# Kernel optimization log

Measured on AMD Instinct MI355X. Metric: run time of the kernel, lower is better.

The kernel has to match this reference:

```python
import jax, jax.numpy as jnp
import numpy as np

H, KV, D, WIN = 16, 4, 128, 1024


def _rope(x, cos, sin):
    # x: [B, H, S, D]; cos/sin: [1, 1, S, D//2]
    d = x.shape[-1] // 2
    x1, x2 = x[..., :d], x[..., d:]
    S = x.shape[2]
    c, s = cos[:, :, :S], sin[:, :, :S]
    return jnp.concatenate([x1 * c + x2 * s, -x1 * s + x2 * c], axis=-1)


def _rms_norm(x):
    eps = jnp.finfo(x.dtype).eps
    return x * jax.lax.rsqrt(jnp.mean(jnp.square(x), axis=-1, keepdims=True) + eps)


def setup_inputs() -> dict:
    key = jax.random.key(0)
    ks = jax.random.split(key, 7)
    B, S, E = 2, 2048, 2048
    return {
        "x": jax.random.normal(ks[0], (B, S, E), jnp.float32),
        "cos": jax.random.normal(ks[1], (1, 1, S, D // 2), jnp.float32),
        "sin": jax.random.normal(ks[2], (1, 1, S, D // 2), jnp.float32),
        "Wq": jax.random.normal(ks[3], (H * D, E), jnp.float32) * 0.02,
        "Wk": jax.random.normal(ks[4], (KV * D, E), jnp.float32) * 0.02,
        "Wv": jax.random.normal(ks[5], (KV * D, E), jnp.float32) * 0.02,
        "Wo": jax.random.normal(ks[6], (E, H * D), jnp.float32) * 0.02,
    }


def reference(x, cos, sin, Wq, Wk, Wv, Wo):
    B, S, E = x.shape
    rep = H // KV
    # projections -> [B, heads, S, D]
    q = (x @ Wq.T).reshape(B, S, H, D).transpose(0, 2, 1, 3)
    k = (x @ Wk.T).reshape(B, S, KV, D).transpose(0, 2, 1, 3)
    v = (x @ Wv.T).reshape(B, S, KV, D).transpose(0, 2, 1, 3)
    # GQA: materialize repeated K/V heads (matches repeat_interleave)
    k = jnp.repeat(k, rep, axis=1)
    v = jnp.repeat(v, rep, axis=1)
    # RoPE then QK RMSNorm (no learned scale)
    q = _rms_norm(_rope(q, cos, sin))
    k = _rms_norm(_rope(k, cos, sin))
    scores = jnp.einsum("bhqd,bhkd->bhqk", q, k) * (D ** -0.5)
    # causal & sliding-window mask
    i = jnp.arange(S)[:, None]
    j = jnp.arange(S)[None, :]
    mask = (i >= j) & (jnp.abs(i - j) < WIN)
    scores = jnp.where(mask[None, None], scores, -jnp.inf)
    attn = jax.nn.softmax(scores, axis=-1)
    out = jnp.einsum("bhqk,bhkd->bhqd", attn, v)
    out = out.transpose(0, 2, 1, 3).reshape(B, S, H * D)
    return out @ Wo.T
```

## Files before the change

### kernel.cpp

```cpp
#include <hip/hip_runtime.h>
#include <stdint.h>

using bf16 = __bf16;
typedef __bf16 bf16x8 __attribute__((ext_vector_type(8)));
typedef __bf16 bf16x4 __attribute__((ext_vector_type(4)));
typedef float f32x4 __attribute__((ext_vector_type(4)));

#define H_ 16
#define KV_ 4
#define D_ 128
#define WIN_ 1024
#define B_ 2
#define S_ 2048
#define E_ 2048
#define HD_ 2048

__device__ __forceinline__ void gld_lds16(const void* gptr, void* lptr) {
    __builtin_amdgcn_global_load_lds(
        (__attribute__((address_space(1))) void*)(uintptr_t)gptr,
        (__attribute__((address_space(3))) void*)(uintptr_t)lptr, 16, 0, 0);
}

__global__ __launch_bounds__(256) void cvt_all(const float* __restrict__ x,
                                               const float* __restrict__ wq,
                                               const float* __restrict__ wk,
                                               const float* __restrict__ wv,
                                               const float* __restrict__ wo,
                                               bf16* __restrict__ dst) {
    int i = (blockIdx.x * 256 + threadIdx.x) * 4;
    const float* src;
    int off;
    if (i < 8388608)       { src = x;  off = 0; }
    else if (i < 12582912) { src = wq; off = 8388608; }
    else if (i < 13631488) { src = wk; off = 12582912; }
    else if (i < 14680064) { src = wv; off = 13631488; }
    else                   { src = wo; off = 14680064; }
    const float4 v = *(const float4*)(src + (i - off));
    bf16x4 o = {(bf16)v.x, (bf16)v.y, (bf16)v.z, (bf16)v.w};
    *(bf16x4*)(dst + i) = o;
}


template <typename OutT>
__global__ __launch_bounds__(256) void gemm_bt(const bf16* __restrict__ A,
                                               const bf16* __restrict__ W,
                                               OutT* __restrict__ C, int K, int ldc) {
    __shared__ alignas(16) bf16 As[128 * 64];
    __shared__ alignas(16) bf16 Bs[128 * 64];
    const int t = threadIdx.x;
    const int lane = t & 63;
    const int wave = t >> 6;
    const int l15 = lane & 15;
    const int quad = lane >> 4;
    const int fsw = l15 & 7;
    const int wm = (wave & 1) * 64;
    const int wn = (wave >> 1) * 64;
    const int m0 = blockIdx.x * 128;
    const int n0 = blockIdx.y * 128;

    f32x4 acc[4][4] = {};

    const int sr = t >> 3;
    const int su = ((t & 7) ^ ((t >> 3) & 7)) * 8;
    const bf16* Ap = A + (size_t)(m0 + sr) * K + su;
    const bf16* Wp = W + (size_t)(n0 + sr) * K + su;

    for (int k0 = 0; k0 < K; k0 += 64) {
#pragma unroll
        for (int c = 0; c < 4; ++c) {
            gld_lds16(Ap + k0 + (size_t)c * 32 * K, &As[c * 2048 + t * 8]);
            gld_lds16(Wp + k0 + (size_t)c * 32 * K, &Bs[c * 2048 + t * 8]);
        }
        __syncthreads();
#pragma unroll
        for (int kh = 0; kh < 2; ++kh) {
            bf16x8 af[4], bfr[4];
#pragma unroll
            for (int i = 0; i < 4; ++i) {
                af[i] = *(const bf16x8*)&As[(wm + i * 16 + l15) * 64 +
                                            (((kh * 4 + quad) ^ fsw) * 8)];
                bfr[i] = *(const bf16x8*)&Bs[(wn + i * 16 + l15) * 64 +
                                             (((kh * 4 + quad) ^ fsw) * 8)];
            }
#pragma unroll
            for (int i = 0; i < 4; ++i)
#pragma unroll
                for (int j = 0; j < 4; ++j)
                    acc[i][j] =
                        __builtin_amdgcn_mfma_f32_16x16x32_bf16(af[i], bfr[j], acc[i][j], 0, 0, 0);
        }
        __syncthreads();
    }
#pragma unroll
    for (int i = 0; i < 4; ++i) {
        const int row = m0 + wm + i * 16 + quad * 4;
#pragma unroll
        for (int j = 0; j < 4; ++j) {
            const int col = n0 + wn + j * 16 + l15;
#pragma unroll
            for (int r = 0; r < 4; ++r) C[(size_t)(row + r) * ldc + col] = (OutT)acc[i][j][r];
        }
    }
}

__global__ __launch_bounds__(256) void gemm_qkv_rope(const bf16* __restrict__ A,
                                                     const bf16* __restrict__ W,
                                                     const float* __restrict__ cosp,
                                                     const float* __restrict__ sinp,
                                                     bf16* __restrict__ qn,
                                                     bf16* __restrict__ kn,
                                                     bf16* __restrict__ vt) {
    __shared__ alignas(16) unsigned char smem[128 * 136 * 2];
    bf16* As = (bf16*)smem;
    bf16* Bs = (bf16*)(smem + 16384);
    bf16* Cs = (bf16*)smem;
    const int t = threadIdx.x;
    const int lane = t & 63;
    const int wave = t >> 6;
    const int l15 = lane & 15;
    const int quad = lane >> 4;
    const int fsw = l15 & 7;
    const int wm = (wave & 1) * 64;
    const int wn = (wave >> 1) * 64;
    const int m0 = blockIdx.x * 128;
    const int n0 = blockIdx.y * 128;
    const int K = E_;

    f32x4 acc[4][4] = {};

    const int sr = t >> 3;
    const int su = ((t & 7) ^ ((t >> 3) & 7)) * 8;
    const bf16* Ap = A + (size_t)(m0 + sr) * K + su;
    const bf16* Wp = W + (size_t)(n0 + sr) * K + su;

    for (int k0 = 0; k0 < K; k0 += 64) {
#pragma unroll
        for (int c = 0; c < 4; ++c) {
            gld_lds16(Ap + k0 + (size_t)c * 32 * K, &As[c * 2048 + t * 8]);
            gld_lds16(Wp + k0 + (size_t)c * 32 * K, &Bs[c * 2048 + t * 8]);
        }
        __syncthreads();
#pragma unroll
        for (int kh = 0; kh < 2; ++kh) {
            bf16x8 af[4], bfr[4];
#pragma unroll
            for (int i = 0; i < 4; ++i) {
                af[i] = *(const bf16x8*)&As[(wm + i * 16 + l15) * 64 +
                                            (((kh * 4 + quad) ^ fsw) * 8)];
                bfr[i] = *(const bf16x8*)&Bs[(wn + i * 16 + l15) * 64 +
                                             (((kh * 4 + quad) ^ fsw) * 8)];
            }
#pragma unroll
            for (int i = 0; i < 4; ++i)
#pragma unroll
                for (int j = 0; j < 4; ++j)
                    acc[i][j] =
                        __builtin_amdgcn_mfma_f32_16x16x32_bf16(af[i], bfr[j], acc[i][j], 0, 0, 0);
        }
        __syncthreads();
    }

#pragma unroll
    for (int i = 0; i < 4; ++i) {
        const int row = wm + i * 16 + quad * 4;
#pragma unroll
        for (int j = 0; j < 4; ++j) {
            const int col = wn + j * 16 + l15;
#pragma unroll
            for (int r = 0; r < 4; ++r) Cs[(row + r) * 136 + col] = (bf16)acc[i][j][r];
        }
    }
    __syncthreads();

    const int unit = n0 >> 7;
    if (unit < 20) {
        const int row = t >> 1;
        const int half = t & 1;
        const int gr = m0 + row;
        const int bb = gr >> 11;
        const int s = gr & 2047;
        const bf16* crow = &Cs[row * 136 + half * 32];
        const float* cp = cosp + s * 64 + half * 32;
        const float* sp = sinp + s * 64 + half * 32;
        bf16x8 xa[4], xb2[4];
#pragma unroll
        for (int u = 0; u < 4; ++u) {
            xa[u] = *(const bf16x8*)(crow + u * 8);
            xb2[u] = *(const bf16x8*)(crow + 64 + u * 8);
        }
        float y1[32], y2[32], ss = 0.0f;
#pragma unroll
        for (int u = 0; u < 4; ++u)
#pragma unroll
            for (int e = 0; e < 8; ++e) {
                const int jj = u * 8 + e;
                const float x1 = (float)xa[u][e];
                const float x2 = (float)xb2[u][e];
                const float c = cp[jj];
                const float sn = sp[jj];
                y1[jj] = x1 * c + x2 * sn;
                y2[jj] = x2 * c - x1 * sn;
                ss += y1[jj] * y1[jj] + y2[jj] * y2[jj];
            }
        ss += __shfl_xor(ss, 1, 64);
        float rr = rsqrtf(ss * (1.0f / 128.0f) + 1.1920929e-7f);
        bf16* dst;
        if (unit < 16) {
            rr *= 0.12751740f;
            dst = qn + ((size_t)(bb * H_ + unit) * S_ + s) * 128 + half * 32;
        } else {
            dst = kn + ((size_t)(bb * KV_ + (unit - 16)) * S_ + s) * 128 + half * 32;
        }
#pragma unroll
        for (int u = 0; u < 4; ++u) {
            bf16x8 p1, p2;
#pragma unroll
            for (int e = 0; e < 8; ++e) {
                p1[e] = (bf16)(y1[u * 8 + e] * rr);
                p2[e] = (bf16)(y2[u * 8 + e] * rr);
            }
            *(bf16x8*)(dst + u * 8) = p1;
            *(bf16x8*)(dst + 64 + u * 8) = p2;
        }
    } else {
        const int jv = unit - 20;
        const int d = t >> 1;
        const int sl0 = (t & 1) * 64;
        const int s0 = (m0 & 2047) + sl0;
        const int bb = m0 >> 11;
        bf16* vdst = vt + ((size_t)(bb * KV_ + jv) * 128 + d) * S_ + s0;
#pragma unroll
        for (int u = 0; u < 8; ++u) {
            bf16x8 pk;
#pragma unroll
            for (int e = 0; e < 8; ++e) pk[e] = Cs[(sl0 + u * 8 + e) * 136 + d];
            *(bf16x8*)(vdst + u * 8) = pk;
        }
    }
}

__global__ __launch_bounds__(256, 4) void attn_fwd(const bf16* __restrict__ Qn,
                                                   const bf16* __restrict__ Kn,
                                                   const bf16* __restrict__ Vt,
                                                   bf16* __restrict__ Out) {
    __shared__ alignas(16) bf16 Ks[64 * 128];
    __shared__ alignas(16) bf16 Vs[128 * 64];
    __shared__ alignas(16) bf16 Ps[4 * 16 * 64];

    const int t = threadIdx.x;
    const int lane = t & 63;
    const int wave = t >> 6;
    const int l15 = lane & 15;
    const int quad = lane >> 4;
    const int swz = l15 & 7;
    const int qb0 = blockIdx.x * 64;
    const int h = blockIdx.y;
    const int b = blockIdx.z;
    const int hk = h >> 2;
    const int qw0 = qb0 + wave * 16;

    const bf16* qbase = Qn + ((size_t)((b * H_ + h) * S_) + qw0 + l15) * 128;
    bf16x8 qf[4];
#pragma unroll
    for (int c4 = 0; c4 < 4; ++c4) qf[c4] = *(const bf16x8*)(qbase + c4 * 32 + quad * 8);

    f32x4 o[8] = {};
    float m = -1e30f, lsum = 0.0f;

    const bf16* kroot = Kn + (size_t)((b * KV_ + hk) * S_) * 128;
    const bf16* vroot = Vt + (size_t)((b * KV_ + hk) * 128) * S_;

    const int ku = (t & 15) ^ ((t >> 4) & 7);
    const int krow = t >> 4;
    const int vu = (t & 7) ^ ((t >> 3) & 7);
    const int vrow = t >> 3;
    const bf16* kst = kroot + (size_t)krow * 128 + ku * 8;
    const bf16* vst = vroot + (size_t)vrow * S_ + vu * 8;
    bf16* ksl = &Ks[t * 8];
    bf16* vsl = &Vs[t * 8];

    int lo = qb0 - (WIN_ - 1);
    if (lo < 0) lo = 0;
    const int kb_start = lo & ~63;
    const int kb_end = qb0 + 64;

    for (int kb = kb_start; kb < kb_end; kb += 64) {
#pragma unroll
        for (int c = 0; c < 4; ++c) gld_lds16(kst + (size_t)(kb + c * 16) * 128, ksl + c * 2048);
#pragma unroll
        for (int c = 0; c < 4; ++c) gld_lds16(vst + (size_t)(c * 32) * S_ + kb, vsl + c * 2048);
        __syncthreads();

        const bool wave_active = (kb + 63 >= qw0 - (WIN_ - 1));
        if (wave_active) {
            f32x4 sacc[4] = {};
#pragma unroll
            for (int kblk = 0; kblk < 4; ++kblk)
#pragma unroll
                for (int c4 = 0; c4 < 4; ++c4) {
                    bf16x8 kf = *(const bf16x8*)&Ks[(kblk * 16 + l15) * 128 +
                                                    (((c4 * 4 + quad) ^ swz) * 8)];
                    sacc[kblk] =
                        __builtin_amdgcn_mfma_f32_16x16x32_bf16(kf, qf[c4], sacc[kblk], 0, 0, 0);
                }

            const int q = qw0 + l15;
            float sv[16];
            const bool interior = (kb + 63 <= qw0) && (kb >= qw0 + 15 - (WIN_ - 1));
            if (interior) {
#pragma unroll
                for (int kblk = 0; kblk < 4; ++kblk)
#pragma unroll
                    for (int r = 0; r < 4; ++r) sv[kblk * 4 + r] = sacc[kblk][r];
            } else {
#pragma unroll
                for (int kblk = 0; kblk < 4; ++kblk)
#pragma unroll
                    for (int r = 0; r < 4; ++r) {
                        const int key = kb + kblk * 16 + quad * 4 + r;
                        const bool valid = (key <= q) && (q - key < WIN_);
                        sv[kblk * 4 + r] = valid ? sacc[kblk][r] : -1e30f;
                    }
            }
            float mc = sv[0];
#pragma unroll
            for (int i = 1; i < 16; ++i) mc = fmaxf(mc, sv[i]);
            mc = fmaxf(mc, __shfl_xor(mc, 16, 64));
            mc = fmaxf(mc, __shfl_xor(mc, 32, 64));
            const float mnew = fmaxf(m, mc);
            const float al = __builtin_amdgcn_exp2f(m - mnew);
            float ls = 0.0f;
#pragma unroll
            for (int i = 0; i < 16; ++i) {
                sv[i] = __builtin_amdgcn_exp2f(sv[i] - mnew);
                ls += sv[i];
            }
            ls += __shfl_xor(ls, 16, 64);
            ls += __shfl_xor(ls, 32, 64);
            lsum = lsum * al + ls;
            m = mnew;
#pragma unroll
            for (int dblk = 0; dblk < 8; ++dblk) o[dblk] *= al;

            bf16* pw = &Ps[wave * 1024 + l15 * 64];
#pragma unroll
            for (int kblk = 0; kblk < 4; ++kblk) {
                bf16x4 pb = {(bf16)sv[kblk * 4 + 0], (bf16)sv[kblk * 4 + 1],
                             (bf16)sv[kblk * 4 + 2], (bf16)sv[kblk * 4 + 3]};
                const int phys = (kblk * 2 + (quad >> 1)) ^ swz;
                *(bf16x4*)&pw[phys * 8 + (quad & 1) * 4] = pb;
            }
#pragma unroll
            for (int kc = 0; kc < 2; ++kc) {
                const int up = ((kc * 4 + quad) ^ swz) * 8;
                bf16x8 pfv = *(const bf16x8*)&pw[up];
#pragma unroll
                for (int dblk = 0; dblk < 8; ++dblk) {
                    bf16x8 vf = *(const bf16x8*)&Vs[(dblk * 16 + l15) * 64 + up];
                    o[dblk] = __builtin_amdgcn_mfma_f32_16x16x32_bf16(vf, pfv, o[dblk], 0, 0, 0);
                }
            }
        }
        __syncthreads();
    }

    const float inv = 1.0f / lsum;
    const int q = qw0 + l15;
    bf16* ob = Out + (size_t)(b * S_ + q) * HD_ + h * 128;
#pragma unroll
    for (int dblk = 0; dblk < 8; ++dblk) {
        bf16x4 ov = {(bf16)(o[dblk][0] * inv), (bf16)(o[dblk][1] * inv),
                     (bf16)(o[dblk][2] * inv), (bf16)(o[dblk][3] * inv)};
        *(bf16x4*)&ob[dblk * 16 + quad * 4] = ov;
    }
}

extern "C" void kernel_launch(void* const* d_in, const int* in_sizes, int n_in, void* d_out,
                              int out_size, void* d_ws, size_t ws_size, hipStream_t stream) {
    const float* x = (const float*)d_in[0];
    const float* cosp = (const float*)d_in[1];
    const float* sinp = (const float*)d_in[2];
    const float* Wq = (const float*)d_in[3];
    const float* Wk = (const float*)d_in[4];
    const float* Wv = (const float*)d_in[5];
    const float* Wo = (const float*)d_in[6];
    float* out = (float*)d_out;

    constexpr size_t MB = 1ull << 20;
    char* ws = (char*)d_ws;
    bf16* xb    = (bf16*)(ws + 0);
    bf16* wqkv  = (bf16*)(ws + 16 * MB);
    bf16* wo    = (bf16*)(ws + 28 * MB);
    bf16* qn    = (bf16*)(ws + 40 * MB);
    bf16* kn    = (bf16*)(ws + 56 * MB);
    bf16* vt    = (bf16*)(ws + 60 * MB);
    bf16* attnb = (bf16*)(ws + 64 * MB);

    cvt_all<<<18432, 256, 0, stream>>>(x, Wq, Wk, Wv, Wo, xb);
    gemm_qkv_rope<<<dim3(32, 24), 256, 0, stream>>>(xb, wqkv, cosp, sinp, qn, kn, vt);
    attn_fwd<<<dim3(32, 16, 2), 256, 0, stream>>>(qn, kn, vt, attnb);
    gemm_bt<float><<<dim3(32, 16), 256, 0, stream>>>(attnb, wo, out, 2048, 2048);
}
```

Before: 289.1 us.

## Rewrite projection GEMMs as 8-wave double-buffered pipelined kernels with larger tiles

Replaces the 128x128 single-buffered QKV and output-projection GEMMs with 512-thread kernels using 256x256 (QKV) and 256x128 (out) tiles. LDS is double-buffered with global-to-LDS loads issued two tiles ahead under explicit vmcnt waits, and MFMA runs in quadrant phases with setprio and sched barriers. Block IDs are swizzled for L2 locality, and the RoPE/RMSNorm/V-transpose epilogue is done in two 128-row chunks. This aims to hide load latency and raise arithmetic intensity. The cost is more LDS per block (128 KB / 96 KB) and heavy register pressure, which limits occupancy.

```diff
diff --git a/kernel.cpp b/kernel.cpp
--- a/kernel.cpp
+++ b/kernel.cpp
@@ -41,200 +41,300 @@
 }
 
 
-template <typename OutT>
-__global__ __launch_bounds__(256) void gemm_bt(const bf16* __restrict__ A,
-                                               const bf16* __restrict__ W,
-                                               OutT* __restrict__ C, int K, int ldc) {
-    __shared__ alignas(16) bf16 As[128 * 64];
-    __shared__ alignas(16) bf16 Bs[128 * 64];
+#define SCHED0() __builtin_amdgcn_sched_barrier(0)
+#define BAR()                          \
+    do {                               \
+        SCHED0();                      \
+        __builtin_amdgcn_s_barrier();  \
+        SCHED0();                      \
+    } while (0)
+#define WAITV(N) asm volatile("s_waitcnt vmcnt(" #N ")" ::: "memory")
+
+#define MMA16(MH, NHI, BF)                                                          \
+    do {                                                                            \
+        __builtin_amdgcn_s_setprio(1);                                              \
+        _Pragma("unroll") for (int i_ = 0; i_ < 4; ++i_) {                          \
+            _Pragma("unroll") for (int j_ = 0; j_ < 2; ++j_) {                      \
+                _Pragma("unroll") for (int kh_ = 0; kh_ < 2; ++kh_) {               \
+                    acc[(MH) * 4 + i_][(NHI) * 2 + j_] =                            \
+                        __builtin_amdgcn_mfma_f32_16x16x32_bf16(                    \
+                            af[i_][kh_], BF[j_][kh_],                               \
+                            acc[(MH) * 4 + i_][(NHI) * 2 + j_], 0, 0, 0);           \
+                }                                                                   \
+            }                                                                       \
+        }                                                                           \
+        __builtin_amdgcn_s_setprio(0);                                              \
+    } while (0)
+
+#define TILE_NH2(TT, AC, BC, DOST, WC)     \
+    do {                                   \
+        rdA(AC, 0);                        \
+        rdB(BC, 0, bf0);                   \
+        BAR();                             \
+        MMA16(0, 0, bf0);                  \
+        BAR();                             \
+        rdB(BC, 1, bf1);                   \
+        BAR();                             \
+        MMA16(0, 1, bf1);                  \
+        BAR();                             \
+        rdA(AC, 1);                        \
+        if (DOST) stB((TT) + 2, BC);       \
+        BAR();                             \
+        MMA16(1, 0, bf0);                  \
+        BAR();                             \
+        if (DOST) stA((TT) + 2, AC);       \
+        BAR();                             \
+        MMA16(1, 1, bf1);                  \
+        SCHED0();                          \
+        if ((WC) == 8) WAITV(8);           \
+        else if ((WC) == 0) WAITV(0);      \
+        BAR();                             \
+    } while (0)
+
+#define TILE_NH1(TT, AC, BC, DOST, WC)     \
+    do {                                   \
+        rdA(AC, 0);                        \
+        rdB(BC, 0, bf0);                   \
+        BAR();                             \
+        MMA16(0, 0, bf0);                  \
+        BAR();                             \
+        rdA(AC, 1);                        \
+        BAR();                             \
+        MMA16(1, 0, bf0);                  \
+        if (DOST) {                        \
+            stB((TT) + 2, BC);             \
+            stA((TT) + 2, AC);             \
+        }                                  \
+        SCHED0();                          \
+        if ((WC) == 6) WAITV(6);           \
+        else if ((WC) == 0) WAITV(0);      \
+        BAR();                             \
+    } while (0)
+
+template <int NH>
+__device__ __forceinline__ void gemm_core(const bf16* __restrict__ A,
+                                          const bf16* __restrict__ W, int K, int m0,
+                                          int n0, bf16* sm, f32x4 (&acc)[8][2 * NH]) {
     const int t = threadIdx.x;
     const int lane = t & 63;
     const int wave = t >> 6;
     const int l15 = lane & 15;
     const int quad = lane >> 4;
-    const int fsw = l15 & 7;
-    const int wm = (wave & 1) * 64;
-    const int wn = (wave >> 1) * 64;
-    const int m0 = blockIdx.x * 128;
-    const int n0 = blockIdx.y * 128;
-
-    f32x4 acc[4][4] = {};
-
-    const int sr = t >> 3;
+    const int fsw8 = (l15 & 7) * 8;
+    const int wm = (wave & 1) * 128;
+    const int wn = (wave >> 1) * (NH * 32);
+    const int nt = K >> 6;
+
+    bf16* const As0 = sm;
+    bf16* const As1 = sm + 16384;
+    bf16* const Bs0 = sm + 32768;
+    bf16* const Bs1 = Bs0 + NH * 8192;
+
     const int su = ((t & 7) ^ ((t >> 3) & 7)) * 8;
-    const bf16* Ap = A + (size_t)(m0 + sr) * K + su;
-    const bf16* Wp = W + (size_t)(n0 + sr) * K + su;
-
-    for (int k0 = 0; k0 < K; k0 += 64) {
-#pragma unroll
-        for (int c = 0; c < 4; ++c) {
-            gld_lds16(Ap + k0 + (size_t)c * 32 * K, &As[c * 2048 + t * 8]);
-            gld_lds16(Wp + k0 + (size_t)c * 32 * K, &Bs[c * 2048 + t * 8]);
-        }
-        __syncthreads();
-#pragma unroll
-        for (int kh = 0; kh < 2; ++kh) {
-            bf16x8 af[4], bfr[4];
-#pragma unroll
-            for (int i = 0; i < 4; ++i) {
-                af[i] = *(const bf16x8*)&As[(wm + i * 16 + l15) * 64 +
-                                            (((kh * 4 + quad) ^ fsw) * 8)];
-                bfr[i] = *(const bf16x8*)&Bs[(wn + i * 16 + l15) * 64 +
-                                             (((kh * 4 + quad) ^ fsw) * 8)];
-            }
-#pragma unroll
-            for (int i = 0; i < 4; ++i)
-#pragma unroll
-                for (int j = 0; j < 4; ++j)
-                    acc[i][j] =
-                        __builtin_amdgcn_mfma_f32_16x16x32_bf16(af[i], bfr[j], acc[i][j], 0, 0, 0);
-        }
-        __syncthreads();
+    const bf16* Ap = A + (size_t)(m0 + (t >> 3)) * K + su;
+    const bf16* Wp = W + (size_t)(n0 + (t >> 3)) * K + su;
+
+    auto stA = [&](int tt, bf16* dst) {
+#pragma unroll
+        for (int c = 0; c < 4; ++c)
+            gld_lds16(Ap + tt * 64 + (size_t)(c * 64) * K, dst + c * 4096 + t * 8);
+    };
+    auto stB = [&](int tt, bf16* dst) {
+#pragma unroll
+        for (int c = 0; c < 2 * NH; ++c)
+            gld_lds16(Wp + tt * 64 + (size_t)(c * 64) * K, dst + c * 4096 + t * 8);
+    };
+
+    bf16x8 af[4][2], bf0[2][2], bf1[2][2];
+    auto rdA = [&](const bf16* S, int mh) {
+#pragma unroll
+        for (int i = 0; i < 4; ++i) {
+            const bf16* r = &S[(wm + mh * 64 + i * 16 + l15) * 64];
+#pragma unroll
+            for (int kh = 0; kh < 2; ++kh)
+                af[i][kh] = *(const bf16x8*)&r[((kh * 4 + quad) * 8) ^ fsw8];
+        }
+    };
+    auto rdB = [&](const bf16* S, int nh, bf16x8 (&f)[2][2]) {
+#pragma unroll
+        for (int j = 0; j < 2; ++j) {
+            const bf16* r = &S[(wn + nh * 32 + j * 16 + l15) * 64];
+#pragma unroll
+            for (int kh = 0; kh < 2; ++kh)
+                f[j][kh] = *(const bf16x8*)&r[((kh * 4 + quad) * 8) ^ fsw8];
+        }
+    };
+
+    stA(0, As0);
+    stB(0, Bs0);
+    stA(1, As1);
+    stB(1, Bs1);
+    SCHED0();
+    if constexpr (NH == 2) WAITV(8);
+    else WAITV(6);
+    BAR();
+
+    if constexpr (NH == 2) {
+        for (int tt = 0; tt < nt - 2; tt += 2) {
+            TILE_NH2(tt, As0, Bs0, 1, 8);
+            TILE_NH2(tt + 1, As1, Bs1, 1, 8);
+        }
+        TILE_NH2(nt - 2, As0, Bs0, 0, 0);
+        TILE_NH2(nt - 1, As1, Bs1, 0, -1);
+    } else {
+        for (int tt = 0; tt < nt - 2; tt += 2) {
+            TILE_NH1(tt, As0, Bs0, 1, 6);
+            TILE_NH1(tt + 1, As1, Bs1, 1, 6);
+        }
+        TILE_NH1(nt - 2, As0, Bs0, 0, 0);
+        TILE_NH1(nt - 1, As1, Bs1, 0, -1);
     }
-#pragma unroll
-    for (int i = 0; i < 4; ++i) {
-        const int row = m0 + wm + i * 16 + quad * 4;
-#pragma unroll
-        for (int j = 0; j < 4; ++j) {
-            const int col = n0 + wn + j * 16 + l15;
-#pragma unroll
-            for (int r = 0; r < 4; ++r) C[(size_t)(row + r) * ldc + col] = (OutT)acc[i][j][r];
-        }
-    }
-}
-
-__global__ __launch_bounds__(256) void gemm_qkv_rope(const bf16* __restrict__ A,
-                                                     const bf16* __restrict__ W,
-                                                     const float* __restrict__ cosp,
-                                                     const float* __restrict__ sinp,
-                                                     bf16* __restrict__ qn,
-                                                     bf16* __restrict__ kn,
-                                                     bf16* __restrict__ vt) {
-    __shared__ alignas(16) unsigned char smem[128 * 136 * 2];
-    bf16* As = (bf16*)smem;
-    bf16* Bs = (bf16*)(smem + 16384);
-    bf16* Cs = (bf16*)smem;
+}
+
+__global__ __launch_bounds__(512, 2) void gemm_qkv8(const bf16* __restrict__ A,
+                                                    const bf16* __restrict__ W,
+                                                    const float* __restrict__ cosp,
+                                                    const float* __restrict__ sinp,
+                                                    bf16* __restrict__ qn,
+                                                    bf16* __restrict__ kn,
+                                                    bf16* __restrict__ vt) {
+    __shared__ alignas(16) bf16 sm[65536];
+    const int flat = blockIdx.y * 16 + blockIdx.x;
+    const int swz = (flat & 7) * 24 + (flat >> 3);
+    const int m0 = (swz & 15) * 256;
+    const int n0 = (swz >> 4) * 256;
+
+    f32x4 acc[8][4] = {};
+    gemm_core<2>(A, W, E_, m0, n0, sm, acc);
+
     const int t = threadIdx.x;
     const int lane = t & 63;
     const int wave = t >> 6;
     const int l15 = lane & 15;
     const int quad = lane >> 4;
-    const int fsw = l15 & 7;
-    const int wm = (wave & 1) * 64;
+    const int wm = (wave & 1) * 128;
     const int wn = (wave >> 1) * 64;
-    const int m0 = blockIdx.x * 128;
-    const int n0 = blockIdx.y * 128;
-    const int K = E_;
-
-    f32x4 acc[4][4] = {};
-
-    const int sr = t >> 3;
-    const int su = ((t & 7) ^ ((t >> 3) & 7)) * 8;
-    const bf16* Ap = A + (size_t)(m0 + sr) * K + su;
-    const bf16* Wp = W + (size_t)(n0 + sr) * K + su;
-
-    for (int k0 = 0; k0 < K; k0 += 64) {
-#pragma unroll
-        for (int c = 0; c < 4; ++c) {
-            gld_lds16(Ap + k0 + (size_t)c * 32 * K, &As[c * 2048 + t * 8]);
-            gld_lds16(Wp + k0 + (size_t)c * 32 * K, &Bs[c * 2048 + t * 8]);
-        }
+    bf16* Cs = sm;
+
+#pragma unroll
+    for (int ch = 0; ch < 2; ++ch) {
         __syncthreads();
-#pragma unroll
-        for (int kh = 0; kh < 2; ++kh) {
-            bf16x8 af[4], bfr[4];
-#pragma unroll
-            for (int i = 0; i < 4; ++i) {
-                af[i] = *(const bf16x8*)&As[(wm + i * 16 + l15) * 64 +
-                                            (((kh * 4 + quad) ^ fsw) * 8)];
-                bfr[i] = *(const bf16x8*)&Bs[(wn + i * 16 + l15) * 64 +
-                                             (((kh * 4 + quad) ^ fsw) * 8)];
-            }
-#pragma unroll
-            for (int i = 0; i < 4; ++i)
-#pragma unroll
-                for (int j = 0; j < 4; ++j)
-                    acc[i][j] =
-                        __builtin_amdgcn_mfma_f32_16x16x32_bf16(af[i], bfr[j], acc[i][j], 0, 0, 0);
+        if (wm == ch * 128) {
+#pragma unroll
+            for (int mi = 0; mi < 8; ++mi) {
+                const int rl = mi * 16 + quad * 4;
+#pragma unroll
+                for (int nf = 0; nf < 4; ++nf) {
+                    const int col = wn + nf * 16 + l15;
+#pragma unroll
+                    for (int r = 0; r < 4; ++r)
+                        Cs[(rl + r) * 264 + col] = (bf16)acc[mi][nf][r];
+                }
+            }
         }
         __syncthreads();
+
+        if (n0 < 2560) {
+            const int rt = t >> 1;
+            const int row = rt & 127;
+            const int hh = rt >> 7;
+            const int half = t & 1;
+            const int gr = m0 + ch * 128 + row;
+            const int bb = gr >> 11;
+            const int s = gr & 2047;
+            const int unit = (n0 >> 7) + hh;
+            const bf16* crow = &Cs[row * 264 + hh * 128 + half * 32];
+            const float* cp = cosp + s * 64 + half * 32;
+            const float* sp = sinp + s * 64 + half * 32;
+            bf16x8 xa[4], xb2[4];
+#pragma unroll
+            for (int u = 0; u < 4; ++u) {
+                xa[u] = *(const bf16x8*)(crow + u * 8);
+                xb2[u] = *(const bf16x8*)(crow + 64 + u * 8);
+            }
+            float y1[32], y2[32], ss = 0.0f;
+#pragma unroll
+            for (int u = 0; u < 4; ++u)
+#pragma unroll
+                for (int e = 0; e < 8; ++e) {
+                    const int jj = u * 8 + e;
+                    const float x1 = (float)xa[u][e];
+                    const float x2 = (float)xb2[u][e];
+                    const float c = cp[jj];
+                    const float sn = sp[jj];
+                    y1[jj] = x1 * c + x2 * sn;
+                    y2[jj] = x2 * c - x1 * sn;
+                    ss += y1[jj] * y1[jj] + y2[jj] * y2[jj];
+                }
+            ss += __shfl_xor(ss, 1, 64);
+            float rr = rsqrtf(ss * (1.0f / 128.0f) + 1.1920929e-7f);
+            bf16* dst;
+            if (unit < 16) {
+                rr *= 0.12751740f;
+                dst = qn + ((size_t)(bb * H_ + unit) * S_ + s) * 128 + half * 32;
+            } else {
+                dst = kn + ((size_t)(bb * KV_ + (unit - 16)) * S_ + s) * 128 + half * 32;
+            }
+#pragma unroll
+            for (int u = 0; u < 4; ++u) {
+                bf16x8 p1, p2;
+#pragma unroll
+                for (int e = 0; e < 8; ++e) {
+                    p1[e] = (bf16)(y1[u * 8 + e] * rr);
+                    p2[e] = (bf16)(y2[u * 8 + e] * rr);
+                }
+                *(bf16x8*)(dst + u * 8) = p1;
+                *(bf16x8*)(dst + 64 + u * 8) = p2;
+            }
+        } else {
+            const int hh = t >> 8;
+            const int d = (t >> 1) & 127;
+            const int sl0 = (t & 1) * 64;
+            const int jv = (n0 >> 7) + hh - 20;
+            const int base = m0 + ch * 128;
+            const int bb = base >> 11;
+            const int sW = (base & 2047) + sl0;
+            bf16* vdst = vt + ((size_t)(bb * KV_ + jv) * 128 + d) * S_ + sW;
+#pragma unroll
+            for (int u = 0; u < 8; ++u) {
+                bf16x8 pk;
+#pragma unroll
+                for (int e = 0; e < 8; ++e)
+                    pk[e] = Cs[(sl0 + u * 8 + e) * 264 + hh * 128 + d];
+                *(bf16x8*)(vdst + u * 8) = pk;
+            }
+        }
     }
-
-#pragma unroll
-    for (int i = 0; i < 4; ++i) {
-        const int row = wm + i * 16 + quad * 4;
-#pragma unroll
-        for (int j = 0; j < 4; ++j) {
-            const int col = wn + j * 16 + l15;
-#pragma unroll
-            for (int r = 0; r < 4; ++r) Cs[(row + r) * 136 + col] = (bf16)acc[i][j][r];
-        }
-    }
-    __syncthreads();
-
-    const int unit = n0 >> 7;
-    if (unit < 20) {
-        const int row = t >> 1;
-        const int half = t & 1;
-        const int gr = m0 + row;
-        const int bb = gr >> 11;
-        const int s = gr & 2047;
-        const bf16* crow = &Cs[row * 136 + half * 32];
-        const float* cp = cosp + s * 64 + half * 32;
-        const float* sp = sinp + s * 64 + half * 32;
-        bf16x8 xa[4], xb2[4];
-#pragma unroll
-        for (int u = 0; u < 4; ++u) {
-            xa[u] = *(const bf16x8*)(crow + u * 8);
-            xb2[u] = *(const bf16x8*)(crow + 64 + u * 8);
-        }
-        float y1[32], y2[32], ss = 0.0f;
-#pragma unroll
-        for (int u = 0; u < 4; ++u)
-#pragma unroll
-            for (int e = 0; e < 8; ++e) {
-                const int jj = u * 8 + e;
-                const float x1 = (float)xa[u][e];
-                const float x2 = (float)xb2[u][e];
-                const float c = cp[jj];
-                const float sn = sp[jj];
-                y1[jj] = x1 * c + x2 * sn;
-                y2[jj] = x2 * c - x1 * sn;
-                ss += y1[jj] * y1[jj] + y2[jj] * y2[jj];
-            }
-        ss += __shfl_xor(ss, 1, 64);
-        float rr = rsqrtf(ss * (1.0f / 128.0f) + 1.1920929e-7f);
-        bf16* dst;
-        if (unit < 16) {
-            rr *= 0.12751740f;
-            dst = qn + ((size_t)(bb * H_ + unit) * S_ + s) * 128 + half * 32;
-        } else {
-            dst = kn + ((size_t)(bb * KV_ + (unit - 16)) * S_ + s) * 128 + half * 32;
-        }
-#pragma unroll
-        for (int u = 0; u < 4; ++u) {
-            bf16x8 p1, p2;
-#pragma unroll
-            for (int e = 0; e < 8; ++e) {
-                p1[e] = (bf16)(y1[u * 8 + e] * rr);
-                p2[e] = (bf16)(y2[u * 8 + e] * rr);
-            }
-            *(bf16x8*)(dst + u * 8) = p1;
-            *(bf16x8*)(dst + 64 + u * 8) = p2;
-        }
-    } else {
-        const int jv = unit - 20;
-        const int d = t >> 1;
-        const int sl0 = (t & 1) * 64;
-        const int s0 = (m0 & 2047) + sl0;
-        const int bb = m0 >> 11;
-        bf16* vdst = vt + ((size_t)(bb * KV_ + jv) * 128 + d) * S_ + s0;
-#pragma unroll
-        for (int u = 0; u < 8; ++u) {
-            bf16x8 pk;
-#pragma unroll
-            for (int e = 0; e < 8; ++e) pk[e] = Cs[(sl0 + u * 8 + e) * 136 + d];
-            *(bf16x8*)(vdst + u * 8) = pk;
+}
+
+__global__ __launch_bounds__(512, 2) void gemm_bt8(const bf16* __restrict__ A,
+                                                   const bf16* __restrict__ W,
+                                                   float* __restrict__ C, int K,
+                                                   int ldc) {
+    __shared__ alignas(16) bf16 sm[49152];
+    const int flat = blockIdx.y * 16 + blockIdx.x;
+    const int swz = (flat & 7) * 32 + (flat >> 3);
+    const int m0 = (swz & 15) * 256;
+    const int n0 = (swz >> 4) * 128;
+
+    f32x4 acc[8][2] = {};
+    gemm_core<1>(A, W, K, m0, n0, sm, acc);
+
+    const int t = threadIdx.x;
+    const int lane = t & 63;
+    const int l15 = lane & 15;
+    const int quad = lane >> 4;
+    const int wave = t >> 6;
+    const int wm = (wave & 1) * 128;
+    const int wn = (wave >> 1) * 32;
+#pragma unroll
+    for (int mi = 0; mi < 8; ++mi) {
+        const int row = m0 + wm + mi * 16 + quad * 4;
+#pragma unroll
+        for (int j = 0; j < 2; ++j) {
+            const int col = n0 + wn + j * 16 + l15;
+#pragma unroll
+            for (int r = 0; r < 4; ++r) C[(size_t)(row + r) * ldc + col] = acc[mi][j][r];
         }
     }
 }
@@ -397,7 +497,7 @@
     bf16* attnb = (bf16*)(ws + 64 * MB);
 
     cvt_all<<<18432, 256, 0, stream>>>(x, Wq, Wk, Wv, Wo, xb);
-    gemm_qkv_rope<<<dim3(32, 24), 256, 0, stream>>>(xb, wqkv, cosp, sinp, qn, kn, vt);
+    gemm_qkv8<<<dim3(16, 12), 512, 0, stream>>>(xb, wqkv, cosp, sinp, qn, kn, vt);
     attn_fwd<<<dim3(32, 16, 2), 256, 0, stream>>>(qn, kn, vt, attnb);
-    gemm_bt<float><<<dim3(32, 16), 256, 0, stream>>>(attnb, wo, out, 2048, 2048);
-}
+    gemm_bt8<<<dim3(16, 16), 512, 0, stream>>>(attnb, wo, out, 2048, 2048);
+}
```

New measurement: 282.1 us. -2.4%, faster.
